# Optimization experiments

Hardware: AMD Instinct MI355X
Metric: run time of the kernel (lower is better)

Reference implementation:

```python
import jax, jax.numpy as jnp
import numpy as np

N = 100_000
E = 1_600_000
D = 128
LN_EPS = 1e-5


def _gcn_layer(x, src, dst, W, b, gamma, beta):
    # GCNConv (PyG defaults): linear transform, add self-loops, symmetric norm,
    # scatter-add aggregation, then bias. Followed by LayerNorm + ReLU.
    n = x.shape[0]
    h = x @ W  # [N, out]
    loop = jnp.arange(n, dtype=src.dtype)
    src_f = jnp.concatenate([src, loop])  # [E+N]
    dst_f = jnp.concatenate([dst, loop])
    deg = jax.ops.segment_sum(jnp.ones(src_f.shape[0], dtype=h.dtype), dst_f, num_segments=n)
    dinv = jnp.where(deg > 0, jax.lax.rsqrt(deg), 0.0)
    norm = dinv[src_f] * dinv[dst_f]  # [E+N]
    msg = h[src_f] * norm[:, None]  # [E+N, out] -- dominant HBM traffic
    out = jax.ops.segment_sum(msg, dst_f, num_segments=n) + b
    # LayerNorm over feature dim
    mu = jnp.mean(out, axis=-1, keepdims=True)
    var = jnp.mean(jnp.square(out - mu), axis=-1, keepdims=True)
    ln = (out - mu) * jax.lax.rsqrt(var + LN_EPS) * gamma + beta
    # ReLU; dropout is identity in eval mode
    return jax.nn.relu(ln)


def setup_inputs() -> dict:
    key = jax.random.key(0)
    ks = jax.random.split(key, 10)
    x = jax.random.normal(ks[0], (N, D), dtype=jnp.float32)
    edge_index = jax.random.randint(ks[1], (2, E), 0, N, dtype=jnp.int32)
    s = 1.0 / np.sqrt(D)
    W1 = jax.random.normal(ks[2], (D, D), dtype=jnp.float32) * s
    b1 = jnp.zeros((D,), dtype=jnp.float32)
    g1 = jnp.ones((D,), dtype=jnp.float32)
    be1 = jnp.zeros((D,), dtype=jnp.float32)
    W2 = jax.random.normal(ks[3], (D, D), dtype=jnp.float32) * s
    b2 = jnp.zeros((D,), dtype=jnp.float32)
    g2 = jnp.ones((D,), dtype=jnp.float32)
    be2 = jnp.zeros((D,), dtype=jnp.float32)
    return {"x": x, "edge_index": edge_index, "W1": W1, "b1": b1, "g1": g1,
            "be1": be1, "W2": W2, "b2": b2, "g2": g2, "be2": be2}


def reference(x, edge_index, W1, b1, g1, be1, W2, b2, g2, be2):
    src, dst = edge_index[0], edge_index[1]  # PyG flow: source_to_target
    h = _gcn_layer(x, src, dst, W1, b1, g1, be1)
    h = _gcn_layer(h, src, dst, W2, b2, g2, be2)
    return h
```

## Files before the change

kernel.cpp:

```cpp
#include <hip/hip_runtime.h>

#define D 128
#define NBSHIFT 9
#define NB (1 << NBSHIFT)
#define PEPB 8192
#define BINS 256
#define CAP 128
#define BCAP 10240

typedef __attribute__((ext_vector_type(8))) short bf16x8;
typedef __attribute__((ext_vector_type(4))) float floatx4;

__device__ __forceinline__ float bflo(unsigned int u){ return __uint_as_float(u << 16); }
__device__ __forceinline__ float bfhi(unsigned int u){ return __uint_as_float(u & 0xffff0000u); }
__device__ __forceinline__ unsigned int f2bfbits(float f){
    unsigned int x = __float_as_uint(f);
    return (x + 0x7fffu + ((x >> 16) & 1u)) >> 16;
}

__global__ __launch_bounds__(512) void k_part(const int* __restrict__ src, const int* __restrict__ dst,
                                              unsigned int* __restrict__ edge1, int* __restrict__ cnt,
                                              int NBK, int NCHUNK, int E){
    __shared__ int lcur[BINS];
    int t = threadIdx.x, blk = blockIdx.x;
    int base = blk * PEPB;
    if (t < BINS) lcur[t] = 0;
    __syncthreads();
#pragma unroll
    for (int j = 0; j < 16; ++j){
        int e = base + j * 512 + t;
        if (e < E){
            int s = src[e], d = dst[e];
            int bk = d >> NBSHIFT;
            int pos = atomicAdd(&lcur[bk], 1);
            if (pos < CAP)
                edge1[((size_t)bk * NCHUNK + blk) * CAP + pos] =
                    (unsigned)s | (((unsigned)d & (NB - 1)) << 20);
        }
    }
    __syncthreads();
    if (t < NBK) cnt[blk * NBK + t] = min(lcur[t], CAP);
}

__global__ __launch_bounds__(512) void k_csr2b(const unsigned int* __restrict__ edge1,
                                               const int* __restrict__ cnt,
                                               int* __restrict__ rowStart, int* __restrict__ rowLen,
                                               float* __restrict__ dinv, int* __restrict__ csr,
                                               int NBK, int NCHUNK, int N){
    __shared__ int cellb[BINS];
    __shared__ unsigned int stage[BCAP];
    __shared__ int hist[NB], sc[NB];
    int b = blockIdx.x, t = threadIdx.x;
    int nbase = b << NBSHIFT;
    int nn = min(N - nbase, NB);

    int v = 0;
    if (t < BINS){ v = (t < NCHUNK) ? cnt[t * NBK + b] : 0; cellb[t] = v; }
    __syncthreads();
    for (int off = 1; off < BINS; off <<= 1){
        int u = 0;
        if (t < BINS && t >= off) u = cellb[t - off];
        __syncthreads();
        if (t < BINS) cellb[t] += u;
        __syncthreads();
    }
    int total = min(cellb[BINS - 1], BCAP);
    __syncthreads();
    if (t < BINS) cellb[t] -= v;
    __syncthreads();

    for (int i = t; i < total; i += 512){
        int lo = 0, hi = BINS - 1;
        while (lo < hi){
            int m = (lo + hi + 1) >> 1;
            if (cellb[m] <= i) lo = m; else hi = m - 1;
        }
        stage[i] = edge1[((size_t)b * NCHUNK + lo) * CAP + (i - cellb[lo])];
    }
    hist[t] = 0;
    __syncthreads();
    for (int i = t; i < total; i += 512) atomicAdd(&hist[stage[i] >> 20], 1);
    __syncthreads();
    sc[t] = hist[t];
    __syncthreads();
    for (int off = 1; off < NB; off <<= 1){
        int u = (t >= off) ? sc[t - off] : 0;
        __syncthreads();
        sc[t] += u;
        __syncthreads();
    }
    {
        int cur = b * BCAP + sc[t] - hist[t];
        sc[t] = cur;
        if (t < nn){
            rowStart[nbase + t] = cur;
            rowLen[nbase + t] = hist[t];
            dinv[nbase + t] = rsqrtf((float)hist[t] + 1.0f);
        }
    }
    __syncthreads();
    for (int i = t; i < total; i += 512){
        unsigned p = stage[i];
        int pos = atomicAdd(&sc[p >> 20], 1);
        csr[pos] = (int)(p & 0xFFFFFu);
    }
}

__global__ __launch_bounds__(256) void k_wtrans(const float* __restrict__ W1,
                                                const float* __restrict__ W2,
                                                unsigned short* __restrict__ Wt1,
                                                unsigned short* __restrict__ Wt2){
    int i = blockIdx.x * 256 + threadIdx.x;
    const float* Ws; unsigned short* Wd; int j = i;
    if (i < 16384){ Ws = W1; Wd = Wt1; } else { Ws = W2; Wd = Wt2; j -= 16384; }
    int k = j >> 7, n = j & 127;
    Wd[n * 128 + k] = (unsigned short)f2bfbits(Ws[k * 128 + n]);
}

template<bool A_BF16>
__global__ __launch_bounds__(256) void k_gemm(const void* __restrict__ Av,
                                              const unsigned short* __restrict__ Wt,
                                              const float* __restrict__ dinv,
                                              unsigned short* __restrict__ Hout, int Nrows){
    int wave = threadIdx.x >> 6, lane = threadIdx.x & 63;
    int m = lane & 15, quad = lane >> 4;
    int row0 = blockIdx.x * 64 + wave * 16;
    int arow = row0 + m;
    int arowc = arow < Nrows ? arow : Nrows - 1;

    bf16x8 a[4];
    if (A_BF16){
        const unsigned short* Ap = (const unsigned short*)Av + (size_t)arowc * D + quad * 8;
#pragma unroll
        for (int kt = 0; kt < 4; ++kt) a[kt] = *(const bf16x8*)(Ap + kt * 32);
    } else {
        const float* Ap = (const float*)Av + (size_t)arowc * D + quad * 8;
#pragma unroll
        for (int kt = 0; kt < 4; ++kt){
            float4 v0 = *(const float4*)(Ap + kt * 32);
            float4 v1 = *(const float4*)(Ap + kt * 32 + 4);
            bf16x8 af;
            af[0] = (short)f2bfbits(v0.x); af[1] = (short)f2bfbits(v0.y);
            af[2] = (short)f2bfbits(v0.z); af[3] = (short)f2bfbits(v0.w);
            af[4] = (short)f2bfbits(v1.x); af[5] = (short)f2bfbits(v1.y);
            af[6] = (short)f2bfbits(v1.z); af[7] = (short)f2bfbits(v1.w);
            a[kt] = af;
        }
    }

    floatx4 acc[8];
#pragma unroll
    for (int nt = 0; nt < 8; ++nt) acc[nt] = (floatx4){0.f, 0.f, 0.f, 0.f};

    const unsigned short* Bp = Wt + m * D + quad * 8;
#pragma unroll
    for (int kt = 0; kt < 4; ++kt){
        bf16x8 bk[8];
#pragma unroll
        for (int nt = 0; nt < 8; ++nt) bk[nt] = *(const bf16x8*)(Bp + nt * 16 * D + kt * 32);
#pragma unroll
        for (int nt = 0; nt < 8; ++nt)
            acc[nt] = __builtin_amdgcn_mfma_f32_16x16x32_bf16(a[kt], bk[nt], acc[nt], 0, 0, 0);
    }
#pragma unroll
    for (int r = 0; r < 4; ++r){
        int rr = row0 + quad * 4 + r;
        if (rr < Nrows){
            float dvr = dinv[rr];
#pragma unroll
            for (int nt = 0; nt < 8; ++nt)
                Hout[(size_t)rr * D + nt * 16 + m] = (unsigned short)f2bfbits(acc[nt][r] * dvr);
        }
    }
}

template<bool OUT_BF16>
__global__ __launch_bounds__(256) void k_agg2(const unsigned short* __restrict__ h,
                                              const int* __restrict__ rowStart,
                                              const int* __restrict__ rowLen,
                                              const int* __restrict__ csr,
                                              const float* __restrict__ dinv,
                                              const float* __restrict__ bias,
                                              const float* __restrict__ gamma,
                                              const float* __restrict__ beta,
                                              void* __restrict__ outv, int N){
    int node = blockIdx.x * 4 + (threadIdx.x >> 6);
    if (node >= N) return;
    int lane = threadIdx.x & 63;
    int half = lane >> 5, li = lane & 31;
    const uint2* hv = (const uint2*)h;

    float dv = dinv[node];
    float4 acc = {0.f, 0.f, 0.f, 0.f};
    if (half == 0){
        uint2 hs = hv[(size_t)node * 32 + li];
        acc.x = bflo(hs.x); acc.y = bfhi(hs.x);
        acc.z = bflo(hs.y); acc.w = bfhi(hs.y);
    }

    int start = rowStart[node], len = rowLen[node], end = start + len;
    int mid = start + ((len + 1) >> 1);
    int i    = half ? mid : start;
    int iend = half ? end : mid;

    for (; i + 4 <= iend; i += 4){
        int s0 = csr[i], s1 = csr[i + 1], s2 = csr[i + 2], s3 = csr[i + 3];
        uint2 h0 = hv[(size_t)s0 * 32 + li];
        uint2 h1 = hv[(size_t)s1 * 32 + li];
        uint2 h2 = hv[(size_t)s2 * 32 + li];
        uint2 h3 = hv[(size_t)s3 * 32 + li];
        acc.x += bflo(h0.x) + bflo(h1.x) + bflo(h2.x) + bflo(h3.x);
        acc.y += bfhi(h0.x) + bfhi(h1.x) + bfhi(h2.x) + bfhi(h3.x);
        acc.z += bflo(h0.y) + bflo(h1.y) + bflo(h2.y) + bflo(h3.y);
        acc.w += bfhi(h0.y) + bfhi(h1.y) + bfhi(h2.y) + bfhi(h3.y);
    }
    for (; i < iend; ++i){
        int s = csr[i];
        uint2 hs = hv[(size_t)s * 32 + li];
        acc.x += bflo(hs.x); acc.y += bfhi(hs.x);
        acc.z += bflo(hs.y); acc.w += bfhi(hs.y);
    }

    acc.x += __shfl_xor(acc.x, 32, 64);
    acc.y += __shfl_xor(acc.y, 32, 64);
    acc.z += __shfl_xor(acc.z, 32, 64);
    acc.w += __shfl_xor(acc.w, 32, 64);

    float4 bb = ((const float4*)bias)[li];
    acc.x = fmaf(acc.x, dv, bb.x); acc.y = fmaf(acc.y, dv, bb.y);
    acc.z = fmaf(acc.z, dv, bb.z); acc.w = fmaf(acc.w, dv, bb.w);

    float s1 = acc.x + acc.y + acc.z + acc.w;
    float s2 = acc.x * acc.x + acc.y * acc.y + acc.z * acc.z + acc.w * acc.w;
#pragma unroll
    for (int off = 16; off > 0; off >>= 1){
        s1 += __shfl_xor(s1, off, 64);
        s2 += __shfl_xor(s2, off, 64);
    }
    float mu = s1 * (1.0f / 128.0f);
    float var = s2 * (1.0f / 128.0f) - mu * mu;
    float rstd = rsqrtf(var + 1e-5f);

    float4 gg = ((const float4*)gamma)[li];
    float4 be = ((const float4*)beta)[li];
    float ox = fmaxf(fmaf((acc.x - mu) * rstd, gg.x, be.x), 0.0f);
    float oy = fmaxf(fmaf((acc.y - mu) * rstd, gg.y, be.y), 0.0f);
    float oz = fmaxf(fmaf((acc.z - mu) * rstd, gg.z, be.z), 0.0f);
    float ow = fmaxf(fmaf((acc.w - mu) * rstd, gg.w, be.w), 0.0f);
    if (half == 0){
        if (OUT_BF16){
            uint2 o;
            o.x = f2bfbits(ox) | (f2bfbits(oy) << 16);
            o.y = f2bfbits(oz) | (f2bfbits(ow) << 16);
            ((uint2*)outv)[(size_t)node * 32 + li] = o;
        } else {
            floatx4 o = {ox, oy, oz, ow};
            __builtin_nontemporal_store(o, (floatx4*)outv + (size_t)node * 32 + li);
        }
    }
}

extern "C" void kernel_launch(void* const* d_in, const int* in_sizes, int n_in,
                              void* d_out, int out_size, void* d_ws, size_t ws_size,
                              hipStream_t stream){
    const float* x   = (const float*)d_in[0];
    const int*   ei  = (const int*)d_in[1];
    const float* W1  = (const float*)d_in[2];
    const float* b1  = (const float*)d_in[3];
    const float* g1  = (const float*)d_in[4];
    const float* be1 = (const float*)d_in[5];
    const float* W2  = (const float*)d_in[6];
    const float* b2  = (const float*)d_in[7];
    const float* g2  = (const float*)d_in[8];
    const float* be2 = (const float*)d_in[9];
    float* out = (float*)d_out;

    const int N = in_sizes[0] / D;
    const int E = in_sizes[1] / 2;
    const int* src = ei;
    const int* dst = ei + E;

    char* w = (char*)d_ws;
    size_t off = 0;
    auto alloc = [&](size_t bytes) -> char* {
        char* p = w + off;
        off = (off + bytes + 255) & ~(size_t)255;
        return p;
    };
    const int NBK = (N + NB - 1) >> NBSHIFT;
    const int NCHUNK = (E + PEPB - 1) / PEPB;
    unsigned int*   edge1    = (unsigned int*)alloc((size_t)NBK * NCHUNK * CAP * 4);
    int*            cnt      = (int*)alloc((size_t)NCHUNK * NBK * 4);
    int*            rowStart = (int*)alloc((size_t)N * 4);
    int*            rowLen   = (int*)alloc((size_t)N * 4);
    float*          dinv     = (float*)alloc((size_t)N * 4);
    int*            csr      = (int*)alloc((size_t)NBK * BCAP * 4);
    unsigned short* wt1      = (unsigned short*)alloc(16384 * 2);
    unsigned short* wt2      = (unsigned short*)alloc(16384 * 2);
    unsigned short* h        = (unsigned short*)alloc((size_t)N * D * 2);
    unsigned short* hmid     = (unsigned short*)d_out;

    int gG = (N + 63) / 64;
    int gA = (N + 3) / 4;

    k_part  <<<NCHUNK, 512, 0, stream>>>(src, dst, edge1, cnt, NBK, NCHUNK, E);
    k_csr2b <<<NBK, 512, 0, stream>>>(edge1, cnt, rowStart, rowLen, dinv, csr, NBK, NCHUNK, N);
    k_wtrans<<<128, 256, 0, stream>>>(W1, W2, wt1, wt2);

    k_gemm<false><<<gG, 256, 0, stream>>>(x, wt1, dinv, h, N);
    k_agg2<true> <<<gA, 256, 0, stream>>>(h, rowStart, rowLen, csr, dinv, b1, g1, be1, hmid, N);
    k_gemm<true> <<<gG, 256, 0, stream>>>(hmid, wt2, dinv, h, N);
    k_agg2<false><<<gA, 256, 0, stream>>>(h, rowStart, rowLen, csr, dinv, b2, g2, be2, out, N);
}
```

Measured before the change: 370.3 us.

## Fuse layer-1 aggregation with layer-2 GEMM and merge weight transpose into partition

The first-layer aggregation plus LayerNorm/ReLU now writes its bf16 tile of 64 nodes into shared memory, and the same block immediately runs the layer-2 MFMA GEMM on it. This removes the intermediate hidden-state round trip through HBM and one kernel launch. The weight transpose is also folded into extra blocks of the partition kernel, and the per-chunk bucket capacity CAP drops from 128 to 96. The trade-offs are fewer, heavier blocks for aggregation: each wave handles 16 nodes sequentially, so there is less latency hiding for the gathers. The smaller CAP also raises the risk of overflowing and dropping edges for skewed degree distributions.

```diff
diff --git a/kernel.cpp b/kernel.cpp
--- a/kernel.cpp
+++ b/kernel.cpp
@@ -5,7 +5,7 @@
 #define NB (1 << NBSHIFT)
 #define PEPB 8192
 #define BINS 256
-#define CAP 128
+#define CAP 96
 #define BCAP 10240
 
 typedef __attribute__((ext_vector_type(8))) short bf16x8;
@@ -18,11 +18,21 @@
     return (x + 0x7fffu + ((x >> 16) & 1u)) >> 16;
 }
 
-__global__ __launch_bounds__(512) void k_part(const int* __restrict__ src, const int* __restrict__ dst,
-                                              unsigned int* __restrict__ edge1, int* __restrict__ cnt,
-                                              int NBK, int NCHUNK, int E){
+__global__ __launch_bounds__(512) void k_partw(const int* __restrict__ src, const int* __restrict__ dst,
+                                               unsigned int* __restrict__ edge1, int* __restrict__ cnt,
+                                               const float* __restrict__ W1, const float* __restrict__ W2,
+                                               unsigned short* __restrict__ wt1, unsigned short* __restrict__ wt2,
+                                               int NBK, int NCHUNK, int E){
+    int blk = blockIdx.x, t = threadIdx.x;
+    if (blk >= NCHUNK){
+        int i = (blk - NCHUNK) * 512 + t;
+        const float* Ws; unsigned short* Wd; int j = i;
+        if (i < 16384){ Ws = W1; Wd = wt1; } else { Ws = W2; Wd = wt2; j -= 16384; }
+        int k = j >> 7, n = j & 127;
+        Wd[n * 128 + k] = (unsigned short)f2bfbits(Ws[k * 128 + n]);
+        return;
+    }
     __shared__ int lcur[BINS];
-    int t = threadIdx.x, blk = blockIdx.x;
     int base = blk * PEPB;
     if (t < BINS) lcur[t] = 0;
     __syncthreads();
@@ -106,22 +116,10 @@
     }
 }
 
-__global__ __launch_bounds__(256) void k_wtrans(const float* __restrict__ W1,
-                                                const float* __restrict__ W2,
-                                                unsigned short* __restrict__ Wt1,
-                                                unsigned short* __restrict__ Wt2){
-    int i = blockIdx.x * 256 + threadIdx.x;
-    const float* Ws; unsigned short* Wd; int j = i;
-    if (i < 16384){ Ws = W1; Wd = Wt1; } else { Ws = W2; Wd = Wt2; j -= 16384; }
-    int k = j >> 7, n = j & 127;
-    Wd[n * 128 + k] = (unsigned short)f2bfbits(Ws[k * 128 + n]);
-}
-
-template<bool A_BF16>
-__global__ __launch_bounds__(256) void k_gemm(const void* __restrict__ Av,
-                                              const unsigned short* __restrict__ Wt,
-                                              const float* __restrict__ dinv,
-                                              unsigned short* __restrict__ Hout, int Nrows){
+__global__ __launch_bounds__(256) void k_gemm1(const float* __restrict__ Av,
+                                               const unsigned short* __restrict__ Wt,
+                                               const float* __restrict__ dinv,
+                                               unsigned short* __restrict__ Hout, int Nrows){
     int wave = threadIdx.x >> 6, lane = threadIdx.x & 63;
     int m = lane & 15, quad = lane >> 4;
     int row0 = blockIdx.x * 64 + wave * 16;
@@ -129,23 +127,17 @@
     int arowc = arow < Nrows ? arow : Nrows - 1;
 
     bf16x8 a[4];
-    if (A_BF16){
-        const unsigned short* Ap = (const unsigned short*)Av + (size_t)arowc * D + quad * 8;
-#pragma unroll
-        for (int kt = 0; kt < 4; ++kt) a[kt] = *(const bf16x8*)(Ap + kt * 32);
-    } else {
-        const float* Ap = (const float*)Av + (size_t)arowc * D + quad * 8;
-#pragma unroll
-        for (int kt = 0; kt < 4; ++kt){
-            float4 v0 = *(const float4*)(Ap + kt * 32);
-            float4 v1 = *(const float4*)(Ap + kt * 32 + 4);
-            bf16x8 af;
-            af[0] = (short)f2bfbits(v0.x); af[1] = (short)f2bfbits(v0.y);
-            af[2] = (short)f2bfbits(v0.z); af[3] = (short)f2bfbits(v0.w);
-            af[4] = (short)f2bfbits(v1.x); af[5] = (short)f2bfbits(v1.y);
-            af[6] = (short)f2bfbits(v1.z); af[7] = (short)f2bfbits(v1.w);
-            a[kt] = af;
-        }
+    const float* Ap = Av + (size_t)arowc * D + quad * 8;
+#pragma unroll
+    for (int kt = 0; kt < 4; ++kt){
+        float4 v0 = *(const float4*)(Ap + kt * 32);
+        float4 v1 = *(const float4*)(Ap + kt * 32 + 4);
+        bf16x8 af;
+        af[0] = (short)f2bfbits(v0.x); af[1] = (short)f2bfbits(v0.y);
+        af[2] = (short)f2bfbits(v0.z); af[3] = (short)f2bfbits(v0.w);
+        af[4] = (short)f2bfbits(v1.x); af[5] = (short)f2bfbits(v1.y);
+        af[6] = (short)f2bfbits(v1.z); af[7] = (short)f2bfbits(v1.w);
+        a[kt] = af;
     }
 
     floatx4 acc[8];
@@ -174,7 +166,128 @@
     }
 }
 
-template<bool OUT_BF16>
+__global__ __launch_bounds__(256) void k_aggemm(const unsigned short* __restrict__ h,
+                                                const int* __restrict__ rowStart,
+                                                const int* __restrict__ rowLen,
+                                                const int* __restrict__ csr,
+                                                const float* __restrict__ dinv,
+                                                const float* __restrict__ bias,
+                                                const float* __restrict__ gamma,
+                                                const float* __restrict__ beta,
+                                                const unsigned short* __restrict__ wt2,
+                                                unsigned short* __restrict__ h2, int N){
+    __shared__ unsigned short hm[64 * 136];
+    int wave = threadIdx.x >> 6, lane = threadIdx.x & 63;
+    int half = lane >> 5, li = lane & 31;
+    int node0 = blockIdx.x * 64;
+    const uint2* hv = (const uint2*)h;
+
+    for (int it = 0; it < 16; ++it){
+        int nl = wave * 16 + it;
+        int node = node0 + nl;
+        if (node < N){
+            float dv = dinv[node];
+            float4 acc = {0.f, 0.f, 0.f, 0.f};
+            if (half == 0){
+                uint2 hs = hv[(size_t)node * 32 + li];
+                acc.x = bflo(hs.x); acc.y = bfhi(hs.x);
+                acc.z = bflo(hs.y); acc.w = bfhi(hs.y);
+            }
+            int start = rowStart[node], len = rowLen[node], end = start + len;
+            int mid = start + ((len + 1) >> 1);
+            int i    = half ? mid : start;
+            int iend = half ? end : mid;
+            for (; i + 4 <= iend; i += 4){
+                int s0 = csr[i], s1 = csr[i + 1], s2 = csr[i + 2], s3 = csr[i + 3];
+                uint2 h0 = hv[(size_t)s0 * 32 + li];
+                uint2 h1 = hv[(size_t)s1 * 32 + li];
+                uint2 h2v = hv[(size_t)s2 * 32 + li];
+                uint2 h3 = hv[(size_t)s3 * 32 + li];
+                acc.x += bflo(h0.x) + bflo(h1.x) + bflo(h2v.x) + bflo(h3.x);
+                acc.y += bfhi(h0.x) + bfhi(h1.x) + bfhi(h2v.x) + bfhi(h3.x);
+                acc.z += bflo(h0.y) + bflo(h1.y) + bflo(h2v.y) + bflo(h3.y);
+                acc.w += bfhi(h0.y) + bfhi(h1.y) + bfhi(h2v.y) + bfhi(h3.y);
+            }
+            for (; i < iend; ++i){
+                int s = csr[i];
+                uint2 hs = hv[(size_t)s * 32 + li];
+                acc.x += bflo(hs.x); acc.y += bfhi(hs.x);
+                acc.z += bflo(hs.y); acc.w += bfhi(hs.y);
+            }
+            acc.x += __shfl_xor(acc.x, 32, 64);
+            acc.y += __shfl_xor(acc.y, 32, 64);
+            acc.z += __shfl_xor(acc.z, 32, 64);
+            acc.w += __shfl_xor(acc.w, 32, 64);
+
+            float4 bb = ((const float4*)bias)[li];
+            acc.x = fmaf(acc.x, dv, bb.x); acc.y = fmaf(acc.y, dv, bb.y);
+            acc.z = fmaf(acc.z, dv, bb.z); acc.w = fmaf(acc.w, dv, bb.w);
+
+            float s1 = acc.x + acc.y + acc.z + acc.w;
+            float s2 = acc.x * acc.x + acc.y * acc.y + acc.z * acc.z + acc.w * acc.w;
+#pragma unroll
+            for (int off = 16; off > 0; off >>= 1){
+                s1 += __shfl_xor(s1, off, 64);
+                s2 += __shfl_xor(s2, off, 64);
+            }
+            float mu = s1 * (1.0f / 128.0f);
+            float var = s2 * (1.0f / 128.0f) - mu * mu;
+            float rstd = rsqrtf(var + 1e-5f);
+
+            float4 gg = ((const float4*)gamma)[li];
+            float4 be = ((const float4*)beta)[li];
+            float ox = fmaxf(fmaf((acc.x - mu) * rstd, gg.x, be.x), 0.0f);
+            float oy = fmaxf(fmaf((acc.y - mu) * rstd, gg.y, be.y), 0.0f);
+            float oz = fmaxf(fmaf((acc.z - mu) * rstd, gg.z, be.z), 0.0f);
+            float ow = fmaxf(fmaf((acc.w - mu) * rstd, gg.w, be.w), 0.0f);
+            if (half == 0){
+                uint2 o;
+                o.x = f2bfbits(ox) | (f2bfbits(oy) << 16);
+                o.y = f2bfbits(oz) | (f2bfbits(ow) << 16);
+                *(uint2*)&hm[nl * 136 + li * 4] = o;
+            }
+        } else {
+            if (half == 0){
+                uint2 z = {0u, 0u};
+                *(uint2*)&hm[nl * 136 + li * 4] = z;
+            }
+        }
+    }
+    __syncthreads();
+
+    int m = lane & 15, quad = lane >> 4;
+    int rowL = wave * 16 + m;
+    bf16x8 a[4];
+#pragma unroll
+    for (int kt = 0; kt < 4; ++kt)
+        a[kt] = *(const bf16x8*)&hm[rowL * 136 + quad * 8 + kt * 32];
+
+    floatx4 acc[8];
+#pragma unroll
+    for (int nt = 0; nt < 8; ++nt) acc[nt] = (floatx4){0.f, 0.f, 0.f, 0.f};
+
+    const unsigned short* Bp = wt2 + m * D + quad * 8;
+#pragma unroll
+    for (int kt = 0; kt < 4; ++kt){
+        bf16x8 bk[8];
+#pragma unroll
+        for (int nt = 0; nt < 8; ++nt) bk[nt] = *(const bf16x8*)(Bp + nt * 16 * D + kt * 32);
+#pragma unroll
+        for (int nt = 0; nt < 8; ++nt)
+            acc[nt] = __builtin_amdgcn_mfma_f32_16x16x32_bf16(a[kt], bk[nt], acc[nt], 0, 0, 0);
+    }
+#pragma unroll
+    for (int r = 0; r < 4; ++r){
+        int rr = node0 + wave * 16 + quad * 4 + r;
+        if (rr < N){
+            float dvr = dinv[rr];
+#pragma unroll
+            for (int nt = 0; nt < 8; ++nt)
+                h2[(size_t)rr * D + nt * 16 + m] = (unsigned short)f2bfbits(acc[nt][r] * dvr);
+        }
+    }
+}
+
 __global__ __launch_bounds__(256) void k_agg2(const unsigned short* __restrict__ h,
                                               const int* __restrict__ rowStart,
                                               const int* __restrict__ rowLen,
@@ -183,7 +296,7 @@
                                               const float* __restrict__ bias,
                                               const float* __restrict__ gamma,
                                               const float* __restrict__ beta,
-                                              void* __restrict__ outv, int N){
+                                              float* __restrict__ outv, int N){
     int node = blockIdx.x * 4 + (threadIdx.x >> 6);
     if (node >= N) return;
     int lane = threadIdx.x & 63;
@@ -248,15 +361,8 @@
     float oz = fmaxf(fmaf((acc.z - mu) * rstd, gg.z, be.z), 0.0f);
     float ow = fmaxf(fmaf((acc.w - mu) * rstd, gg.w, be.w), 0.0f);
     if (half == 0){
-        if (OUT_BF16){
-            uint2 o;
-            o.x = f2bfbits(ox) | (f2bfbits(oy) << 16);
-            o.y = f2bfbits(oz) | (f2bfbits(ow) << 16);
-            ((uint2*)outv)[(size_t)node * 32 + li] = o;
-        } else {
-            floatx4 o = {ox, oy, oz, ow};
-            __builtin_nontemporal_store(o, (floatx4*)outv + (size_t)node * 32 + li);
-        }
+        floatx4 o = {ox, oy, oz, ow};
+        __builtin_nontemporal_store(o, (floatx4*)outv + (size_t)node * 32 + li);
     }
 }
 
@@ -298,17 +404,14 @@
     unsigned short* wt1      = (unsigned short*)alloc(16384 * 2);
     unsigned short* wt2      = (unsigned short*)alloc(16384 * 2);
     unsigned short* h        = (unsigned short*)alloc((size_t)N * D * 2);
-    unsigned short* hmid     = (unsigned short*)d_out;
+    unsigned short* h2       = (unsigned short*)alloc((size_t)N * D * 2);
 
     int gG = (N + 63) / 64;
     int gA = (N + 3) / 4;
 
-    k_part  <<<NCHUNK, 512, 0, stream>>>(src, dst, edge1, cnt, NBK, NCHUNK, E);
+    k_partw <<<NCHUNK + 64, 512, 0, stream>>>(src, dst, edge1, cnt, W1, W2, wt1, wt2, NBK, NCHUNK, E);
     k_csr2b <<<NBK, 512, 0, stream>>>(edge1, cnt, rowStart, rowLen, dinv, csr, NBK, NCHUNK, N);
-    k_wtrans<<<128, 256, 0, stream>>>(W1, W2, wt1, wt2);
-
-    k_gemm<false><<<gG, 256, 0, stream>>>(x, wt1, dinv, h, N);
-    k_agg2<true> <<<gA, 256, 0, stream>>>(h, rowStart, rowLen, csr, dinv, b1, g1, be1, hmid, N);
-    k_gemm<true> <<<gG, 256, 0, stream>>>(hmid, wt2, dinv, h, N);
-    k_agg2<false><<<gA, 256, 0, stream>>>(h, rowStart, rowLen, csr, dinv, b2, g2, be2, out, N);
-}
+    k_gemm1 <<<gG, 256, 0, stream>>>(x, wt1, dinv, h, N);
+    k_aggemm<<<gG, 256, 0, stream>>>(h, rowStart, rowLen, csr, dinv, b1, g1, be1, wt2, h2, N);
+    k_agg2  <<<gA, 256, 0, stream>>>(h2, rowStart, rowLen, csr, dinv, b2, g2, be2, out, N);
+}
```

After: 418.9 us. +13.1%, slower.
